# Performance work log

Hardware: AMD Instinct MI355X
Metric: run time of the kernel (lower is better)

## Reference

```python
import jax, jax.numpy as jnp
import numpy as np

T, B, N_INP, N_HID, N_OUT = 512, 512, 64, 768, 64
DT = 0.01


def setup_inputs() -> dict:
    key = jax.random.key(0)
    k = jax.random.split(key, 7)
    d_in = N_INP + 2 * N_HID  # 1600, concat(x, hz, hy)
    s = lambda fan_in: 1.0 / np.sqrt(fan_in)
    return {
        "x": jax.random.normal(k[0], (T, B, N_INP), dtype=jnp.float32),
        "W_h": jax.random.uniform(k[1], (N_HID, d_in), jnp.float32, -s(d_in), s(d_in)),
        "b_h": jax.random.uniform(k[2], (N_HID,), jnp.float32, -s(d_in), s(d_in)),
        "W_p": jax.random.uniform(k[3], (N_HID, d_in), jnp.float32, -s(d_in), s(d_in)),
        "b_p": jax.random.uniform(k[4], (N_HID,), jnp.float32, -s(d_in), s(d_in)),
        "W_r": jax.random.uniform(k[5], (N_OUT, N_HID), jnp.float32, -s(N_HID), s(N_HID)),
        "b_r": jax.random.uniform(k[6], (N_OUT,), jnp.float32, -s(N_HID), s(N_HID)),
    }


def reference(x, W_h, b_h, W_p, b_p, W_r, b_r):
    dt = jnp.asarray(DT, x.dtype)

    def step(carry, xt):
        hy, hz, hp = carry
        # |.|**2 == square for real inputs
        sq = jnp.concatenate([jnp.square(xt), jnp.square(hz), jnp.square(hy)], axis=1)
        hp = jnp.tanh(sq @ W_p.T + b_p)
        lin = jnp.concatenate([xt, hz, hy], axis=1)
        hz = hz + dt * (jnp.tanh(lin @ W_h.T + b_h) + hp)
        hy = hy + dt * hz
        return (hy, hz, hp), None

    h0 = jnp.zeros((x.shape[1], N_HID), x.dtype)
    (hy, hz, hp), _ = jax.lax.scan(step, (h0, h0, h0), x)
    return hy @ W_r.T + b_r
```

## Files before the change

### kernel.cpp

```cpp
#include <hip/hip_runtime.h>
#include <hip/hip_fp16.h>

typedef _Float16 f16x8 __attribute__((ext_vector_type(8)));
typedef float f32x4 __attribute__((ext_vector_type(4)));
typedef float f32x16 __attribute__((ext_vector_type(16)));
typedef unsigned short u16;
typedef unsigned int u32;

#define T_STEPS 512
#define BATCH   512
#define DTF     0.01f

#define CTR_OFF 0
#define CTR_SZ  1048576
#define WB_OFF  (CTR_OFF + CTR_SZ)
#define WB_SZ   (32*200*384*2)
#define WRB_OFF (WB_OFF + WB_SZ)
#define WRB_SZ  (4*24*64*8*2)
#define ST_OFF  (WRB_OFF + WRB_SZ)
#define ST_SZ   (2*8*64*1536*2)
#define WS_NEED (ST_OFF + ST_SZ)

#define MFMA32(a,b,c) __builtin_amdgcn_mfma_f32_32x32x16_f16((a),(b),(c),0,0,0)
#define MFMA16(a,b,c) __builtin_amdgcn_mfma_f32_16x16x32_f16((a),(b),(c),0,0,0)

#define ACQUIRE_L1() asm volatile("s_waitcnt vmcnt(0)\n\tbuffer_inv sc0" ::: "memory")

__device__ __forceinline__ u16 f2h(float f){ _Float16 h = (_Float16)f; return *reinterpret_cast<u16*>(&h); }
__device__ __forceinline__ float h2f(u16 u){ _Float16 h = *reinterpret_cast<_Float16*>(&u); return (float)h; }

__device__ __forceinline__ float ftanh(float x){
  float a = fminf(fmaxf(x, -12.f), 12.f);
  float e = __expf(2.f * a);
  return 1.f - 2.f * __builtin_amdgcn_rcpf(e + 1.f);
}


__global__ __launch_bounds__(64) void prep_weights(const float* __restrict__ Wh,
                                                   const float* __restrict__ Wp,
                                                   const float* __restrict__ Wr,
                                                   u16* __restrict__ Wb, u16* __restrict__ Wrb){
  int b = blockIdx.x, l = threadIdx.x;
  if (b < 6400){
    int s = b / 200, r2 = b % 200;
    int m2 = r2 / 100, u = r2 % 100;
    if (l < 48){
      int c = l >> 1, kh = l & 1;
      int gg = c*2 + kh, rr = gg >> 3, cc = gg & 7;
      size_t dst = (size_t)s*76800 + (size_t)(m2*100 + u)*384 + (size_t)rr*64 + (size_t)((cc ^ (rr & 7))*8);
      const float* W = m2 ? Wp : Wh;
      const float* src = W + (size_t)(s*24 + c)*1600 + u*16 + kh*8;
      f16x8 o;
#pragma unroll
      for (int e = 0; e < 8; ++e) o[e] = (_Float16)src[e];
      *reinterpret_cast<f16x8*>(Wb + dst) = o;
    }
  } else {
    int b2 = b - 6400;
    int nt = b2 / 24, kt = b2 % 24;
    int c = nt*16 + (l & 15), k = kt*32 + (l >> 4)*8;
    const float* src = Wr + (size_t)c*768 + k;
    f16x8 o;
#pragma unroll
    for (int e = 0; e < 8; ++e) o[e] = (_Float16)src[e];
    *reinterpret_cast<f16x8*>(Wrb + ((size_t)b2*64 + l)*8) = o;
  }
}

__global__ __launch_bounds__(256, 1) void rnn_main(
    const float* __restrict__ x, const float* __restrict__ bh_g, const float* __restrict__ bp_g,
    const float* __restrict__ br_g, const u16* __restrict__ Wb, const u16* __restrict__ Wrb,
    u16* __restrict__ st, u32* __restrict__ ctr, float* __restrict__ out)
{
  extern __shared__ u16 smem[];
  __shared__ int s_dead, s_slot, s_xcd;

  const int tid = threadIdx.x;
  if (tid == 0){
    s_dead = 0;
    u32 xcd;
    asm volatile("s_getreg_b32 %0, hwreg(HW_REG_XCC_ID)" : "=s"(xcd));
    xcd &= 7u;
    s_xcd  = (int)xcd;
    s_slot = (int)atomicAdd(ctr + xcd, 1u);
  }
  __syncthreads();
  const int gx = s_xcd;
  const int s  = s_slot;
  if (s >= 32) return;

  const int c0   = s * 24;
  const int l    = tid & 63;
  const int w    = tid >> 6;
  const int m    = w & 1;
  const int p    = w >> 1;
  const int colW = l & 31;
  const int khB  = l >> 5;
  const bool validC = (colW < 24);
  const int colB = validC ? colW : colW - 24;
  const int gran = colB*2 + khB;
  const int grr  = gran >> 3, gcc = gran & 7;
  const int bfi  = grr*8 + (gcc ^ (grr & 7));

  u32* FL = ctr + 2048 + (size_t)gx*16384;

  {
    const float4* srcw = reinterpret_cast<const float4*>(Wb + (size_t)s*76800);
    float4* dst = reinterpret_cast<float4*>(smem);
    for (int i = tid; i < 9600; i += 256) dst[i] = srcw[i];
  }
  __syncthreads();

  const f16x8* WBp = reinterpret_cast<const f16x8*>(smem);
  u16* scr16 = smem + 76800;

  f16x8 xbh[4], xbp[4];
  if (p == 0){
#pragma unroll
    for (int u = 0; u < 4; ++u){ xbh[u] = WBp[u*48 + bfi]; xbp[u] = WBp[(100+u)*48 + bfi]; }
  }

  const int dcol = c0 + (validC ? colW : 0);
  float bhv = 0.f, bpv = 0.f;
  if (w < 2){ bhv = bh_g[dcol]; bpv = bp_g[dcol]; }

  float hz[16] = {}, hy[16] = {};

  auto wait_flags = [&](u32 tgt){
    if (s_dead) return;
    long spins = 0;
    for (;;){
      bool ok = true;
      if (l < 32) ok = (__hip_atomic_load(FL + l*32, __ATOMIC_RELAXED, __HIP_MEMORY_SCOPE_AGENT) >= tgt);
      if (__all(ok)) break;
      __builtin_amdgcn_s_sleep(1);
      if (++spins > 1000000L){ if (l == 0) s_dead = 1; break; }
    }
  };

#define STATE_LOOP(U0c, NUc) do { \
    f16x8 av[4]; \
    _Pragma("unroll") \
    for (int i = 0; i < 4; ++i) av[i] = *reinterpret_cast<const f16x8*>(stb + (size_t)((U0c)-4+i)*16); \
    _Pragma("unroll") \
    for (int i = 0; i < (NUc); ++i){ \
      f16x8 a = av[i & 3]; \
      if (i + 4 < (NUc)) av[i & 3] = *reinterpret_cast<const f16x8*>(stb + (size_t)((U0c)+i)*16); \
      f16x8 bh8 = WBp[((U0c)+i)*48 + bfi]; \
      f16x8 bp8 = WBp[(100+(U0c)+i)*48 + bfi]; \
      f16x8 asq = a*a; \
      accH = MFMA32(a,   bh8, accH); \
      accP = MFMA32(asq, bp8, accP); \
    } } while (0)

#pragma unroll 1
  for (int t = 0; t < T_STEPS; ++t){
    f32x16 accH = {}, accP = {};

    if (p == 0){
      const float* xb = x + ((size_t)t*BATCH + gx*64 + m*32 + colW)*64 + khB*8;
#pragma unroll
      for (int u = 0; u < 4; ++u){
        const float4 uu = *reinterpret_cast<const float4*>(xb + u*16);
        const float4 vv = *reinterpret_cast<const float4*>(xb + u*16 + 4);
        f16x8 xa8, xs8;
        xa8[0]=(_Float16)uu.x; xa8[1]=(_Float16)uu.y; xa8[2]=(_Float16)uu.z; xa8[3]=(_Float16)uu.w;
        xa8[4]=(_Float16)vv.x; xa8[5]=(_Float16)vv.y; xa8[6]=(_Float16)vv.z; xa8[7]=(_Float16)vv.w;
        xs8[0]=(_Float16)(uu.x*uu.x); xs8[1]=(_Float16)(uu.y*uu.y); xs8[2]=(_Float16)(uu.z*uu.z); xs8[3]=(_Float16)(uu.w*uu.w);
        xs8[4]=(_Float16)(vv.x*vv.x); xs8[5]=(_Float16)(vv.y*vv.y); xs8[6]=(_Float16)(vv.z*vv.z); xs8[7]=(_Float16)(vv.w*vv.w);
        accH = MFMA32(xa8, xbh[u], accH);
        accP = MFMA32(xs8, xbp[u], accP);
      }
    }

    if (w == 0){
      if (t > 0) wait_flags((u32)t);
      ACQUIRE_L1();
    }
    __syncthreads();
    if (s_dead) break;

    const u16* stb = st + ((((size_t)(t&1)*8 + gx)*64) + m*32 + colW)*1536 + khB*8;
    if (p == 0) STATE_LOOP(4, 46); else STATE_LOOP(50, 50);

    if (p == 1){
#pragma unroll
      for (int e = 0; e < 16; ++e){
        scr16[(m*2+0)*1024 + e*64 + l] = f2h(accH[e]);
        scr16[(m*2+1)*1024 + e*64 + l] = f2h(accP[e]);
      }
    }
    __syncthreads();

    if (p == 0){
      u16* wtb = st + (((size_t)((t+1)&1)*8 + gx)*64)*1536;
#pragma unroll
      for (int e = 0; e < 16; ++e){
        float aH = accH[e] + h2f(scr16[(m*2+0)*1024 + e*64 + l]);
        float aP = accP[e] + h2f(scr16[(m*2+1)*1024 + e*64 + l]);
        float hv = ftanh(aH + bhv);
        float pv = ftanh(aP + bpv);
        hz[e] += DTF * (hv + pv);
        hy[e] += DTF * hz[e];
        if (validC){
          int row = m*32 + (e & 3) + 8*(e >> 2) + 4*khB;
          wtb[(size_t)row*1536 + dcol]       = f2h(hz[e]);
          wtb[(size_t)row*1536 + 768 + dcol] = f2h(hy[e]);
        }
      }
      asm volatile("s_waitcnt vmcnt(0)" ::: "memory");
    }
    __syncthreads();
    if (tid == 0)
      __hip_atomic_store(FL + s*32, (u32)(t+1), __ATOMIC_RELAXED, __HIP_MEMORY_SCOPE_AGENT);
  }
#undef STATE_LOOP

  if (s == 0 && !s_dead){
    if (w == 0){ wait_flags((u32)T_STEPS); ACQUIRE_L1(); }
    __syncthreads();
    if (!s_dead){
      const int colL = l & 15, kq4 = l >> 4;
      const u16* hyb = st + (((size_t)gx*64) + w*16 + colL)*1536 + 768 + kq4*8;
      const f16x8* Wr8 = reinterpret_cast<const f16x8*>(Wrb);
      f32x4 oc[4] = {};
#pragma unroll
      for (int kt = 0; kt < 24; ++kt){
        f16x8 a = *reinterpret_cast<const f16x8*>(hyb + (size_t)kt*32);
#pragma unroll
        for (int nt = 0; nt < 4; ++nt)
          oc[nt] = MFMA16(a, Wr8[(nt*24 + kt)*64 + l], oc[nt]);
      }
      const int rowC = w*16 + kq4*4;
#pragma unroll
      for (int nt = 0; nt < 4; ++nt){
        float bb = br_g[nt*16 + colL];
#pragma unroll
        for (int e = 0; e < 4; ++e)
          out[(size_t)(gx*64 + rowC + e)*64 + nt*16 + colL] = oc[nt][e] + bb;
      }
    }
  }
}

extern "C" void kernel_launch(void* const* d_in, const int* in_sizes, int n_in,
                              void* d_out, int out_size, void* d_ws, size_t ws_size,
                              hipStream_t stream) {
  const float* x  = (const float*)d_in[0];
  const float* Wh = (const float*)d_in[1];
  const float* bh = (const float*)d_in[2];
  const float* Wp = (const float*)d_in[3];
  const float* bp = (const float*)d_in[4];
  const float* Wr = (const float*)d_in[5];
  const float* br = (const float*)d_in[6];
  float* out = (float*)d_out;

  if (ws_size < (size_t)WS_NEED) return;
  char* ws = (char*)d_ws;

  u16* Wb  = (u16*)(ws + WB_OFF);
  u16* Wrb = (u16*)(ws + WRB_OFF);
  u16* st  = (u16*)(ws + ST_OFF);
  u32* ctr = (u32*)(ws + CTR_OFF);

  hipMemsetAsync(ws + CTR_OFF, 0, CTR_SZ, stream);
  hipMemsetAsync(ws + ST_OFF,  0, ST_SZ,  stream);

  prep_weights<<<6496, 64, 0, stream>>>(Wh, Wp, Wr, Wb, Wrb);

  (void)hipFuncSetAttribute(reinterpret_cast<const void*>(rnn_main),
                            hipFuncAttributeMaxDynamicSharedMemorySize, 161792);
  rnn_main<<<256, 256, 161792, stream>>>(x, bh, bp, br, Wb, Wrb, st, ctr, out);
}
```

Before: 7.262 ms.

## Split recurrent epilogue across both K-halves and deepen state prefetch

The elementwise tanh/state-update epilogue, previously done only by the p==0 warps, is now split so each K-half warp group finalizes half of the 16 accumulator rows. Each exchanges the other half through shared scratch, which halves per-warp epilogue work and the hz/hy register state. The state-load prefetch ring in the inner MFMA loop also grows from 4 to 8 vectors to hide more global-load latency. The cost is more live registers for the prefetch buffer, and the scratch exchange now goes in both directions.

```diff
diff --git a/kernel.cpp b/kernel.cpp
--- a/kernel.cpp
+++ b/kernel.cpp
@@ -121,10 +121,10 @@
   }
 
   const int dcol = c0 + (validC ? colW : 0);
-  float bhv = 0.f, bpv = 0.f;
-  if (w < 2){ bhv = bh_g[dcol]; bpv = bp_g[dcol]; }
-
-  float hz[16] = {}, hy[16] = {};
+  const float bhv = bh_g[dcol];
+  const float bpv = bp_g[dcol];
+
+  float hz[8] = {}, hy[8] = {};
 
   auto wait_flags = [&](u32 tgt){
     if (s_dead) return;
@@ -139,13 +139,13 @@
   };
 
 #define STATE_LOOP(U0c, NUc) do { \
-    f16x8 av[4]; \
+    f16x8 av[8]; \
     _Pragma("unroll") \
-    for (int i = 0; i < 4; ++i) av[i] = *reinterpret_cast<const f16x8*>(stb + (size_t)((U0c)-4+i)*16); \
+    for (int i = 0; i < 8; ++i) av[i] = *reinterpret_cast<const f16x8*>(stb + (size_t)((U0c)-4+i)*16); \
     _Pragma("unroll") \
     for (int i = 0; i < (NUc); ++i){ \
-      f16x8 a = av[i & 3]; \
-      if (i + 4 < (NUc)) av[i & 3] = *reinterpret_cast<const f16x8*>(stb + (size_t)((U0c)+i)*16); \
+      f16x8 a = av[i & 7]; \
+      if (i + 8 < (NUc)) av[i & 7] = *reinterpret_cast<const f16x8*>(stb + (size_t)((U0c)+i+4)*16); \
       f16x8 bh8 = WBp[((U0c)+i)*48 + bfi]; \
       f16x8 bp8 = WBp[(100+(U0c)+i)*48 + bfi]; \
       f16x8 asq = a*a; \
@@ -183,33 +183,36 @@
     const u16* stb = st + ((((size_t)(t&1)*8 + gx)*64) + m*32 + colW)*1536 + khB*8;
     if (p == 0) STATE_LOOP(4, 46); else STATE_LOOP(50, 50);
 
-    if (p == 1){
-#pragma unroll
-      for (int e = 0; e < 16; ++e){
-        scr16[(m*2+0)*1024 + e*64 + l] = f2h(accH[e]);
-        scr16[(m*2+1)*1024 + e*64 + l] = f2h(accP[e]);
-      }
-    }
-    __syncthreads();
-
-    if (p == 0){
+    {
+      const int po = 1 - p;
+#pragma unroll
+      for (int eo = 0; eo < 8; ++eo){
+        const int e = po*8 + eo;
+        scr16[((m*2+po)*2+0)*512 + eo*64 + l] = f2h(accH[e]);
+        scr16[((m*2+po)*2+1)*512 + eo*64 + l] = f2h(accP[e]);
+      }
+    }
+    __syncthreads();
+
+    {
       u16* wtb = st + (((size_t)((t+1)&1)*8 + gx)*64)*1536;
 #pragma unroll
-      for (int e = 0; e < 16; ++e){
-        float aH = accH[e] + h2f(scr16[(m*2+0)*1024 + e*64 + l]);
-        float aP = accP[e] + h2f(scr16[(m*2+1)*1024 + e*64 + l]);
+      for (int eo = 0; eo < 8; ++eo){
+        const int e = p*8 + eo;
+        float aH = accH[e] + h2f(scr16[((m*2+p)*2+0)*512 + eo*64 + l]);
+        float aP = accP[e] + h2f(scr16[((m*2+p)*2+1)*512 + eo*64 + l]);
         float hv = ftanh(aH + bhv);
         float pv = ftanh(aP + bpv);
-        hz[e] += DTF * (hv + pv);
-        hy[e] += DTF * hz[e];
+        hz[eo] += DTF * (hv + pv);
+        hy[eo] += DTF * hz[eo];
         if (validC){
           int row = m*32 + (e & 3) + 8*(e >> 2) + 4*khB;
-          wtb[(size_t)row*1536 + dcol]       = f2h(hz[e]);
-          wtb[(size_t)row*1536 + 768 + dcol] = f2h(hy[e]);
+          wtb[(size_t)row*1536 + dcol]       = f2h(hz[eo]);
+          wtb[(size_t)row*1536 + 768 + dcol] = f2h(hy[eo]);
         }
       }
-      asm volatile("s_waitcnt vmcnt(0)" ::: "memory");
-    }
+    }
+    asm volatile("s_waitcnt vmcnt(0)" ::: "memory");
     __syncthreads();
     if (tid == 0)
       __hip_atomic_store(FL + s*32, (u32)(t+1), __ATOMIC_RELAXED, __HIP_MEMORY_SCOPE_AGENT);
```

Result: no change. 7.213 ms (-0.7%).
